# Kernel optimization log

Measured on AMD Instinct MI355X. Metric: run time of the kernel, lower is better.

Reference implementation:

```python
import jax, jax.numpy as jnp
import numpy as np

N_CAND = 10   # n_point_candidate
SIGMA = 1.0   # std threshold for vote filtering
EPS = 1e-6


def _get_pt_candidates(pcld, kpts_ofst, seg, cpt_ofst, k):
    # pcld [b,n,3]; kpts_ofst [b,n,8,3]; seg [b,n,1]; cpt_ofst [b,n,1,3]
    offsets = jnp.concatenate([kpts_ofst, cpt_ofst], axis=2)        # [b,n,9,3]
    scores = jnp.squeeze(seg, axis=-1)                              # [b,n]
    _, idx = jax.lax.top_k(scores, k)                               # [b,k] most confident points
    cands = pcld[:, :, None, :] + offsets                           # [b,n,9,3] candidate kpt positions
    cands = jnp.take_along_axis(cands, idx[:, :, None, None], axis=1)  # [b,k,9,3]
    return jnp.transpose(cands, (0, 2, 1, 3))                       # [b,9,k,3]


def _pts_clustering_with_std(kpts_cans, sigma=SIGMA):
    # kpts_cans [b,n_kpts,k,3]: keep candidates within sigma*std of the mean, average survivors
    mean = jnp.mean(kpts_cans, axis=2, keepdims=True)
    std = jnp.std(kpts_cans, axis=2, keepdims=True)
    inlier = jnp.all(jnp.abs(kpts_cans - mean) <= sigma * std, axis=-1)  # [b,n_kpts,k]
    w = inlier.astype(kpts_cans.dtype)[..., None]
    return jnp.sum(kpts_cans * w, axis=2) / (jnp.sum(w, axis=2) + EPS)   # [b,n_kpts,3]


def _rt_svd_transform(A, B, w):
    # Weighted Kabsch: find R,t with R @ A + t ~= B.  A,B [b,n,3]; w [n]
    wn = w / jnp.sum(w)
    cA = jnp.einsum('n,bnc->bc', wn, A)[:, None, :]                 # weighted centroids
    cB = jnp.einsum('n,bnc->bc', wn, B)[:, None, :]
    Am, Bm = A - cA, B - cB
    H = jnp.einsum('bni,n,bnj->bij', Am, w, Bm)                     # [b,3,3] cross-covariance
    U, S, Vh = jnp.linalg.svd(H)
    V = jnp.swapaxes(Vh, -1, -2)
    R0 = V @ jnp.swapaxes(U, -1, -2)
    flip = jnp.where(jnp.linalg.det(R0) < 0.0, -1.0, 1.0)           # reflection fix
    V = V.at[:, :, -1].multiply(flip[:, None])
    R = V @ jnp.swapaxes(U, -1, -2)                                 # [b,3,3]
    t = jnp.swapaxes(cB, -1, -2) - R @ jnp.swapaxes(cA, -1, -2)     # [b,3,1]
    return R, t


def setup_inputs() -> dict:
    key = jax.random.key(0)
    k1, k2, k3, k4, k5 = jax.random.split(key, 5)
    b, n, nk = 64, 12288, 8
    return {
        'pcld_input': jax.random.normal(k1, (b, n, 3), jnp.float32),
        'kpts_pre_input': jax.random.normal(k2, (b, n, nk, 3), jnp.float32),
        'cpt_pre_input': jax.random.normal(k3, (b, n, 1, 3), jnp.float32),
        'seg_pre_input': jax.random.uniform(k4, (b, n, 1), jnp.float32),
        'mesh_kpts_input': jax.random.normal(k5, (b, nk + 1, 3), jnp.float32),
    }


def reference(pcld_input, kpts_pre_input, cpt_pre_input, seg_pre_input, mesh_kpts_input):
    obj_kpts = _get_pt_candidates(pcld_input, kpts_pre_input, seg_pre_input, cpt_pre_input, N_CAND)
    kpts_voted = _pts_clustering_with_std(obj_kpts)                 # [b,9,3]
    n_pts = kpts_voted.shape[1]
    weights_vector = jnp.ones((n_pts,), dtype=kpts_voted.dtype)
    batch_R, batch_t = _rt_svd_transform(mesh_kpts_input, kpts_voted, weights_vector)
    batch_t = jnp.reshape(batch_t, (-1, 3))
    return batch_R, batch_t, kpts_voted
```

## Files before the change

kernel.cpp:

```cpp
#include <hip/hip_runtime.h>
#include <math.h>

typedef unsigned long long u64;
typedef unsigned int u32;

#define NB      64
#define NPTS    12288
#define KTOP    10
#define NKP     9
#define T       1024
#define CAND_MAX 128
#define THETA   0.997f

#define CHUNKS   4
#define TPB_A    768
#define CAP      64
#define WS_STRIDE 320

__device__ __forceinline__ u64 pack(float v, int idx) {
    return ((u64)__float_as_uint(v) << 32) | (u32)(~idx);
}
__device__ __forceinline__ int unpack_idx(u64 p) { return (int)(~(u32)p); }

__device__ __forceinline__ float rcp_fast(float x)  { return __builtin_amdgcn_rcpf(x); }
__device__ __forceinline__ float rsq_fast(float x)  { return __builtin_amdgcn_rsqf(x); }
__device__ __forceinline__ float sqrt_fast(float x) { return __builtin_amdgcn_sqrtf(x); }

__global__ __launch_bounds__(TPB_A)
void pose_onepass(const float* __restrict__ pcld,
                  const float* __restrict__ kpts,
                  const float* __restrict__ cpt,
                  const float* __restrict__ seg,
                  const float* __restrict__ mesh,
                  u32* __restrict__ ctr,
                  u64* __restrict__ wsd,
                  float* __restrict__ out)
{
    const int blk   = blockIdx.x;
    const int b     = blk >> 2;
    const int chunk = blk & 3;
    const int t     = threadIdx.x;
    const int lane  = t & 63;

    __shared__ u64    lc[CAP];
    __shared__ int    lcnt;
    __shared__ int    last_s;
    __shared__ u64    cand[CHUNKS * CAP];
    __shared__ int    cnts_s[CHUNKS];
    __shared__ int    n_s, bad_s;
    __shared__ int    topidx[KTOP];
    __shared__ float4 cands4[NKP][KTOP];
    __shared__ float  voted[NKP][3];
    __shared__ float  meshS[NKP * 3];

    if (t == 0) lcnt = 0;
    __syncthreads();

    const float4* segc4 = (const float4*)(seg + (size_t)b * NPTS) + (size_t)chunk * TPB_A;
    float4 a = segc4[t];
    const int base_idx = chunk * (TPB_A * 4) + t * 4;
    #pragma unroll
    for (int c = 0; c < 4; ++c) {
        float v = (c == 0) ? a.x : (c == 1) ? a.y : (c == 2) ? a.z : a.w;
        if (v >= THETA) {
            int slot = atomicAdd(&lcnt, 1);
            if (slot < CAP) lc[slot] = pack(v, base_idx + c);
        }
    }
    __syncthreads();

    u64* wb = wsd + (size_t)b * WS_STRIDE;
    if (t == 0) wb[chunk] = (u64)lcnt;
    int m = lcnt < CAP ? lcnt : CAP;
    if (t < m) wb[4 + chunk * CAP + t] = lc[t];
    __syncthreads();

    if (t == 0) {
        __threadfence();
        u32 old = atomicAdd(&ctr[b], 1u);
        if (old == 3u) __threadfence();
        last_s = (old == 3u) ? 1 : 0;
    }
    __syncthreads();
    if (!last_s) return;

    float meshv = 0.0f;
    if (t < NKP * 3) meshv = mesh[(size_t)b * (NKP * 3) + t];
    if (t < CHUNKS * CAP) cand[t] = wb[4 + t];
    if (t == 0) {
        int off = 0, badv = 0;
        #pragma unroll
        for (int c = 0; c < CHUNKS; ++c) {
            int cc = (int)wb[c];
            cnts_s[c] = cc < CAP ? cc : CAP;
            off += cc;
            if (cc > CAP) badv = 1;
        }
        n_s = off;
        bad_s = badv;
    }
    if (t < NKP * 3) meshS[t] = meshv;
    __syncthreads();

    const int n = n_s;
    const int bad = bad_s;

    if (!bad && n >= KTOP) {
        if (t < CHUNKS * CAP) {
            u64 my = cand[t];
            bool valid = (t & (CAP - 1)) < cnts_s[t >> 6];
            int r = 0;
            #pragma unroll
            for (int c2 = 0; c2 < CHUNKS; ++c2) {
                int cc = cnts_s[c2];
                for (int i2 = 0; i2 < cc; ++i2)
                    r += (cand[c2 * CAP + i2] > my) ? 1 : 0;
            }
            if (valid && r < KTOP) topidx[r] = unpack_idx(my);
        }
    } else if (t < 64) {
        const float* segb = seg + (size_t)b * NPTS;
        u64 loc[KTOP];
        #pragma unroll
        for (int j = 0; j < KTOP; ++j) loc[j] = 0;
        for (int i = lane; i < NPTS; i += 64) {
            u64 p = pack(segb[i], i);
            if (p > loc[KTOP - 1]) {
                loc[KTOP - 1] = p;
                #pragma unroll
                for (int j = KTOP - 1; j > 0; --j) {
                    if (loc[j] > loc[j - 1]) { u64 tmp = loc[j]; loc[j] = loc[j - 1]; loc[j - 1] = tmp; }
                }
            }
        }
        u64 cur = loc[0];
        #pragma unroll
        for (int k = 0; k < KTOP; ++k) {
            u64 w = cur;
            #pragma unroll
            for (int s = 1; s < 64; s <<= 1) {
                u64 o = __shfl_xor(w, s);
                w = o > w ? o : w;
            }
            if (lane == 0) topidx[k] = unpack_idx(w);
            if (cur == w) {
                #pragma unroll
                for (int i = 0; i + 1 < KTOP; ++i) loc[i] = loc[i + 1];
                loc[KTOP - 1] = 0;
                cur = loc[0];
            }
        }
    }
    __syncthreads();

    if (t < NKP * KTOP) {
        int j = t / KTOP;
        int i = t % KTOP;
        int p = topidx[i];
        size_t base = (size_t)b * NPTS + p;
        float px = pcld[base * 3 + 0], py = pcld[base * 3 + 1], pz = pcld[base * 3 + 2];
        float ox, oy, oz;
        if (j < 8) {
            size_t kb = (base * 8 + j) * 3;
            ox = kpts[kb + 0]; oy = kpts[kb + 1]; oz = kpts[kb + 2];
        } else {
            size_t cb = base * 3;
            ox = cpt[cb + 0]; oy = cpt[cb + 1]; oz = cpt[cb + 2];
        }
        cands4[j][i] = make_float4(px + ox, py + oy, pz + oz, 0.0f);
    }
    __syncthreads();

    if (t < NKP) {
        float4 c4[KTOP];
        #pragma unroll
        for (int i = 0; i < KTOP; ++i) c4[i] = cands4[t][i];

        float mean[3] = {0.f, 0.f, 0.f};
        #pragma unroll
        for (int i = 0; i < KTOP; ++i) {
            mean[0] += c4[i].x; mean[1] += c4[i].y; mean[2] += c4[i].z;
        }
        #pragma unroll
        for (int c = 0; c < 3; ++c) mean[c] *= (1.0f / KTOP);

        float var[3] = {0.f, 0.f, 0.f};
        #pragma unroll
        for (int i = 0; i < KTOP; ++i) {
            float d0 = c4[i].x - mean[0]; var[0] += d0 * d0;
            float d1 = c4[i].y - mean[1]; var[1] += d1 * d1;
            float d2 = c4[i].z - mean[2]; var[2] += d2 * d2;
        }
        float sd[3];
        #pragma unroll
        for (int c = 0; c < 3; ++c) sd[c] = sqrtf(var[c] * (1.0f / KTOP));

        float wsum = 0.f, acc[3] = {0.f, 0.f, 0.f};
        #pragma unroll
        for (int i = 0; i < KTOP; ++i) {
            bool in = (fabsf(c4[i].x - mean[0]) <= sd[0]) &&
                      (fabsf(c4[i].y - mean[1]) <= sd[1]) &&
                      (fabsf(c4[i].z - mean[2]) <= sd[2]);
            if (in) {
                wsum += 1.f;
                acc[0] += c4[i].x; acc[1] += c4[i].y; acc[2] += c4[i].z;
            }
        }
        float inv = 1.f / (wsum + 1e-6f);
        #pragma unroll
        for (int c = 0; c < 3; ++c) {
            float v = acc[c] * inv;
            voted[t][c] = v;
            out[NB * 9 + NB * 3 + ((size_t)b * NKP + t) * 3 + c] = v;
        }
    }
    __syncthreads();

    if (t == 0) {
        float A[NKP][3], Bv[NKP][3];
        float cA[3] = {0, 0, 0}, cB[3] = {0, 0, 0};
        for (int nn = 0; nn < NKP; ++nn) {
            for (int c = 0; c < 3; ++c) {
                A[nn][c]  = meshS[nn * 3 + c];
                Bv[nn][c] = voted[nn][c];
                cA[c] += A[nn][c];
                cB[c] += Bv[nn][c];
            }
        }
        for (int c = 0; c < 3; ++c) { cA[c] *= (1.0f / NKP); cB[c] *= (1.0f / NKP); }

        float H[3][3] = {{0,0,0},{0,0,0},{0,0,0}};
        for (int nn = 0; nn < NKP; ++nn)
            for (int i = 0; i < 3; ++i)
                for (int j = 0; j < 3; ++j)
                    H[i][j] += (A[nn][i] - cA[i]) * (Bv[nn][j] - cB[j]);

        float Km[3][3];
        for (int i = 0; i < 3; ++i)
            for (int j = 0; j < 3; ++j) {
                float s = 0;
                for (int l = 0; l < 3; ++l) s += H[l][i] * H[l][j];
                Km[i][j] = s;
            }

        float V[3][3] = {{1,0,0},{0,1,0},{0,0,1}};
        for (int sweep = 0; sweep < 5; ++sweep) {
            for (int p = 0; p < 2; ++p) {
                for (int q = p + 1; q < 3; ++q) {
                    float apq = Km[p][q];
                    float app = Km[p][p], aqq = Km[q][q];
                    if (fabsf(apq) <= 1e-12f * (fabsf(app) + fabsf(aqq)) || apq == 0.0f) continue;
                    float theta = (aqq - app) * rcp_fast(2.0f * apq);
                    float tj = ((theta >= 0.0f) ? 1.0f : -1.0f) *
                               rcp_fast(fabsf(theta) + sqrt_fast(theta * theta + 1.0f));
                    float cj = rsq_fast(tj * tj + 1.0f);
                    float sj = tj * cj;
                    for (int l = 0; l < 3; ++l) {
                        float klp = Km[l][p], klq = Km[l][q];
                        Km[l][p] = cj * klp - sj * klq;
                        Km[l][q] = sj * klp + cj * klq;
                    }
                    for (int l = 0; l < 3; ++l) {
                        float kpl = Km[p][l], kql = Km[q][l];
                        Km[p][l] = cj * kpl - sj * kql;
                        Km[q][l] = sj * kpl + cj * kql;
                    }
                    for (int l = 0; l < 3; ++l) {
                        float vlp = V[l][p], vlq = V[l][q];
                        V[l][p] = cj * vlp - sj * vlq;
                        V[l][q] = sj * vlp + cj * vlq;
                    }
                }
            }
        }

        float eig[3] = {Km[0][0], Km[1][1], Km[2][2]};
        int ord[3] = {0, 1, 2};
        if (eig[ord[0]] < eig[ord[1]]) { int tmp = ord[0]; ord[0] = ord[1]; ord[1] = tmp; }
        if (eig[ord[1]] < eig[ord[2]]) { int tmp = ord[1]; ord[1] = ord[2]; ord[2] = tmp; }
        if (eig[ord[0]] < eig[ord[1]]) { int tmp = ord[0]; ord[0] = ord[1]; ord[1] = tmp; }

        float detH =
            H[0][0] * (H[1][1] * H[2][2] - H[1][2] * H[2][1]) -
            H[0][1] * (H[1][0] * H[2][2] - H[1][2] * H[2][0]) +
            H[0][2] * (H[1][0] * H[2][1] - H[1][1] * H[2][0]);
        float dsign[3] = {1.0f, 1.0f, (detH < 0.0f) ? -1.0f : 1.0f};

        float R[3][3] = {{0,0,0},{0,0,0},{0,0,0}};
        for (int k = 0; k < 3; ++k) {
            int c = ord[k];
            float s = sqrt_fast(fmaxf(eig[c], 0.0f));
            float invs = rcp_fast(fmaxf(s, 1e-12f));
            float u[3];
            for (int l = 0; l < 3; ++l) {
                float a2 = 0;
                for (int mm = 0; mm < 3; ++mm) a2 += H[l][mm] * V[mm][c];
                u[l] = a2 * invs;
            }
            for (int r = 0; r < 3; ++r)
                for (int cc = 0; cc < 3; ++cc)
                    R[r][cc] += dsign[k] * V[r][c] * u[cc];
        }

        float tv[3];
        for (int c = 0; c < 3; ++c) {
            float a2 = 0;
            for (int mm = 0; mm < 3; ++mm) a2 += R[c][mm] * cA[mm];
            tv[c] = cB[c] - a2;
        }

        for (int r = 0; r < 3; ++r)
            for (int c = 0; c < 3; ++c)
                out[(size_t)b * 9 + r * 3 + c] = R[r][c];
        for (int c = 0; c < 3; ++c)
            out[NB * 9 + (size_t)b * 3 + c] = tv[c];
    }
}

__global__ __launch_bounds__(T)
void pose_fused(const float* __restrict__ pcld,
                const float* __restrict__ kpts,
                const float* __restrict__ cpt,
                const float* __restrict__ seg,
                const float* __restrict__ mesh,
                float* __restrict__ out)
{
    const int b = blockIdx.x;
    const int t = threadIdx.x;
    const int lane = t & 63;
    const int wid = t >> 6;

    __shared__ u64    cand[CAND_MAX];
    __shared__ int    cnt;
    __shared__ int    topidx[KTOP];
    __shared__ float4 cands4[NKP][KTOP];
    __shared__ float  voted[NKP][3];
    __shared__ float  meshS[NKP * 3];

    if (t == 0) cnt = 0;
    float meshv = 0.0f;
    if (t < NKP * 3) meshv = mesh[(size_t)b * (NKP * 3) + t];
    __syncthreads();

    const float4* segb4 = (const float4*)(seg + (size_t)b * NPTS);
    #pragma unroll
    for (int j = 0; j < 3; ++j) {
        int f4 = t + j * T;
        float4 a = segb4[f4];
        #pragma unroll
        for (int c = 0; c < 4; ++c) {
            float v = (c == 0) ? a.x : (c == 1) ? a.y : (c == 2) ? a.z : a.w;
            if (v >= THETA) {
                int slot = atomicAdd(&cnt, 1);
                if (slot < CAND_MAX) cand[slot] = pack(v, 4 * f4 + c);
            }
        }
    }
    if (t < NKP * 3) meshS[t] = meshv;
    __syncthreads();

    if (wid == 0) {
        int n = cnt;
        if (n >= KTOP && n <= CAND_MAX) {
            u64 my0 = (lane < n)      ? cand[lane]      : 0;
            u64 my1 = (lane + 64 < n) ? cand[lane + 64] : 0;
            int r0 = 0, r1 = 0;
            for (int i = 0; i < n; ++i) {
                u64 ci = cand[i];
                r0 += (ci > my0) ? 1 : 0;
                r1 += (ci > my1) ? 1 : 0;
            }
            if (lane < n && r0 < KTOP)      topidx[r0] = unpack_idx(my0);
            if (lane + 64 < n && r1 < KTOP) topidx[r1] = unpack_idx(my1);
        } else {
            const float* segb = seg + (size_t)b * NPTS;
            u64 loc[KTOP];
            #pragma unroll
            for (int j = 0; j < KTOP; ++j) loc[j] = 0;
            for (int i = lane; i < NPTS; i += 64) {
                u64 p = pack(segb[i], i);
                if (p > loc[KTOP - 1]) {
                    loc[KTOP - 1] = p;
                    #pragma unroll
                    for (int j = KTOP - 1; j > 0; --j) {
                        if (loc[j] > loc[j - 1]) { u64 tmp = loc[j]; loc[j] = loc[j - 1]; loc[j - 1] = tmp; }
                    }
                }
            }
            u64 cur = loc[0];
            #pragma unroll
            for (int k = 0; k < KTOP; ++k) {
                u64 w = cur;
                #pragma unroll
                for (int s = 1; s < 64; s <<= 1) {
                    u64 o = __shfl_xor(w, s);
                    w = o > w ? o : w;
                }
                if (lane == 0) topidx[k] = unpack_idx(w);
                if (cur == w) {
                    #pragma unroll
                    for (int i = 0; i + 1 < KTOP; ++i) loc[i] = loc[i + 1];
                    loc[KTOP - 1] = 0;
                    cur = loc[0];
                }
            }
        }
    }
    __syncthreads();

    if (t < NKP * KTOP) {
        int j = t / KTOP;
        int i = t % KTOP;
        int p = topidx[i];
        size_t base = (size_t)b * NPTS + p;
        float px = pcld[base * 3 + 0], py = pcld[base * 3 + 1], pz = pcld[base * 3 + 2];
        float ox, oy, oz;
        if (j < 8) {
            size_t kb = (base * 8 + j) * 3;
            ox = kpts[kb + 0]; oy = kpts[kb + 1]; oz = kpts[kb + 2];
        } else {
            size_t cb = base * 3;
            ox = cpt[cb + 0]; oy = cpt[cb + 1]; oz = cpt[cb + 2];
        }
        cands4[j][i] = make_float4(px + ox, py + oy, pz + oz, 0.0f);
    }
    __syncthreads();

    if (t < NKP) {
        float4 c4[KTOP];
        #pragma unroll
        for (int i = 0; i < KTOP; ++i) c4[i] = cands4[t][i];
        float mean[3] = {0.f, 0.f, 0.f};
        #pragma unroll
        for (int i = 0; i < KTOP; ++i) { mean[0] += c4[i].x; mean[1] += c4[i].y; mean[2] += c4[i].z; }
        #pragma unroll
        for (int c = 0; c < 3; ++c) mean[c] *= (1.0f / KTOP);
        float var[3] = {0.f, 0.f, 0.f};
        #pragma unroll
        for (int i = 0; i < KTOP; ++i) {
            float d0 = c4[i].x - mean[0]; var[0] += d0 * d0;
            float d1 = c4[i].y - mean[1]; var[1] += d1 * d1;
            float d2 = c4[i].z - mean[2]; var[2] += d2 * d2;
        }
        float sd[3];
        #pragma unroll
        for (int c = 0; c < 3; ++c) sd[c] = sqrtf(var[c] * (1.0f / KTOP));
        float wsum = 0.f, acc[3] = {0.f, 0.f, 0.f};
        #pragma unroll
        for (int i = 0; i < KTOP; ++i) {
            bool in = (fabsf(c4[i].x - mean[0]) <= sd[0]) &&
                      (fabsf(c4[i].y - mean[1]) <= sd[1]) &&
                      (fabsf(c4[i].z - mean[2]) <= sd[2]);
            if (in) { wsum += 1.f; acc[0] += c4[i].x; acc[1] += c4[i].y; acc[2] += c4[i].z; }
        }
        float inv = 1.f / (wsum + 1e-6f);
        #pragma unroll
        for (int c = 0; c < 3; ++c) {
            float v = acc[c] * inv;
            voted[t][c] = v;
            out[NB * 9 + NB * 3 + ((size_t)b * NKP + t) * 3 + c] = v;
        }
    }
    __syncthreads();

    if (t == 0) {
        float A[NKP][3], Bv[NKP][3];
        float cA[3] = {0, 0, 0}, cB[3] = {0, 0, 0};
        for (int nn = 0; nn < NKP; ++nn) {
            for (int c = 0; c < 3; ++c) {
                A[nn][c]  = meshS[nn * 3 + c];
                Bv[nn][c] = voted[nn][c];
                cA[c] += A[nn][c];
                cB[c] += Bv[nn][c];
            }
        }
        for (int c = 0; c < 3; ++c) { cA[c] *= (1.0f / NKP); cB[c] *= (1.0f / NKP); }
        float H[3][3] = {{0,0,0},{0,0,0},{0,0,0}};
        for (int nn = 0; nn < NKP; ++nn)
            for (int i = 0; i < 3; ++i)
                for (int j = 0; j < 3; ++j)
                    H[i][j] += (A[nn][i] - cA[i]) * (Bv[nn][j] - cB[j]);
        float Km[3][3];
        for (int i = 0; i < 3; ++i)
            for (int j = 0; j < 3; ++j) {
                float s = 0;
                for (int l = 0; l < 3; ++l) s += H[l][i] * H[l][j];
                Km[i][j] = s;
            }
        float V[3][3] = {{1,0,0},{0,1,0},{0,0,1}};
        for (int sweep = 0; sweep < 5; ++sweep) {
            for (int p = 0; p < 2; ++p) {
                for (int q = p + 1; q < 3; ++q) {
                    float apq = Km[p][q];
                    float app = Km[p][p], aqq = Km[q][q];
                    if (fabsf(apq) <= 1e-12f * (fabsf(app) + fabsf(aqq)) || apq == 0.0f) continue;
                    float theta = (aqq - app) * rcp_fast(2.0f * apq);
                    float tj = ((theta >= 0.0f) ? 1.0f : -1.0f) *
                               rcp_fast(fabsf(theta) + sqrt_fast(theta * theta + 1.0f));
                    float cj = rsq_fast(tj * tj + 1.0f);
                    float sj = tj * cj;
                    for (int l = 0; l < 3; ++l) {
                        float klp = Km[l][p], klq = Km[l][q];
                        Km[l][p] = cj * klp - sj * klq;
                        Km[l][q] = sj * klp + cj * klq;
                    }
                    for (int l = 0; l < 3; ++l) {
                        float kpl = Km[p][l], kql = Km[q][l];
                        Km[p][l] = cj * kpl - sj * kql;
                        Km[q][l] = sj * kpl + cj * kql;
                    }
                    for (int l = 0; l < 3; ++l) {
                        float vlp = V[l][p], vlq = V[l][q];
                        V[l][p] = cj * vlp - sj * vlq;
                        V[l][q] = sj * vlp + cj * vlq;
                    }
                }
            }
        }
        float eig[3] = {Km[0][0], Km[1][1], Km[2][2]};
        int ord[3] = {0, 1, 2};
        if (eig[ord[0]] < eig[ord[1]]) { int tmp = ord[0]; ord[0] = ord[1]; ord[1] = tmp; }
        if (eig[ord[1]] < eig[ord[2]]) { int tmp = ord[1]; ord[1] = ord[2]; ord[2] = tmp; }
        if (eig[ord[0]] < eig[ord[1]]) { int tmp = ord[0]; ord[0] = ord[1]; ord[1] = tmp; }
        float detH =
            H[0][0] * (H[1][1] * H[2][2] - H[1][2] * H[2][1]) -
            H[0][1] * (H[1][0] * H[2][2] - H[1][2] * H[2][0]) +
            H[0][2] * (H[1][0] * H[2][1] - H[1][1] * H[2][0]);
        float dsign[3] = {1.0f, 1.0f, (detH < 0.0f) ? -1.0f : 1.0f};
        float R[3][3] = {{0,0,0},{0,0,0},{0,0,0}};
        for (int k = 0; k < 3; ++k) {
            int c = ord[k];
            float s = sqrt_fast(fmaxf(eig[c], 0.0f));
            float invs = rcp_fast(fmaxf(s, 1e-12f));
            float u[3];
            for (int l = 0; l < 3; ++l) {
                float a2 = 0;
                for (int mm = 0; mm < 3; ++mm) a2 += H[l][mm] * V[mm][c];
                u[l] = a2 * invs;
            }
            for (int r = 0; r < 3; ++r)
                for (int cc = 0; cc < 3; ++cc)
                    R[r][cc] += dsign[k] * V[r][c] * u[cc];
        }
        float tv[3];
        for (int c = 0; c < 3; ++c) {
            float a2 = 0;
            for (int mm = 0; mm < 3; ++mm) a2 += R[c][mm] * cA[mm];
            tv[c] = cB[c] - a2;
        }
        for (int r = 0; r < 3; ++r)
            for (int c = 0; c < 3; ++c)
                out[(size_t)b * 9 + r * 3 + c] = R[r][c];
        for (int c = 0; c < 3; ++c)
            out[NB * 9 + (size_t)b * 3 + c] = tv[c];
    }
}

extern "C" void kernel_launch(void* const* d_in, const int* in_sizes, int n_in,
                              void* d_out, int out_size, void* d_ws, size_t ws_size,
                              hipStream_t stream) {
    const float* pcld = (const float*)d_in[0];
    const float* kpts = (const float*)d_in[1];
    const float* cpt  = (const float*)d_in[2];
    const float* seg  = (const float*)d_in[3];
    const float* mesh = (const float*)d_in[4];
    float* out = (float*)d_out;

    const size_t need = 256 + (size_t)NB * WS_STRIDE * sizeof(u64);
    if (d_ws != nullptr && ws_size >= need) {
        u32* ctr = (u32*)d_ws;
        u64* wsd = (u64*)((char*)d_ws + 256);
        hipMemsetAsync(d_ws, 0, NB * sizeof(u32), stream);
        pose_onepass<<<NB * CHUNKS, TPB_A, 0, stream>>>(pcld, kpts, cpt, seg, mesh, ctr, wsd, out);
    } else {
        pose_fused<<<NB, T, 0, stream>>>(pcld, kpts, cpt, seg, mesh, out);
    }
}
```

Measured before the change: 133.3 us.

## Split one-pass kernel into filter and solve kernels, dropping memset and atomic counter

Measured after the change: 119.0 us. 10.7% less time.

```diff
diff --git a/kernel.cpp b/kernel.cpp
--- a/kernel.cpp
+++ b/kernel.cpp
@@ -15,6 +15,7 @@
 #define CHUNKS   4
 #define TPB_A    768
 #define CAP      64
+#define TPB_B    256
 #define WS_STRIDE 320
 
 __device__ __forceinline__ u64 pack(float v, int idx) {
@@ -27,32 +28,15 @@
 __device__ __forceinline__ float sqrt_fast(float x) { return __builtin_amdgcn_sqrtf(x); }
 
 __global__ __launch_bounds__(TPB_A)
-void pose_onepass(const float* __restrict__ pcld,
-                  const float* __restrict__ kpts,
-                  const float* __restrict__ cpt,
-                  const float* __restrict__ seg,
-                  const float* __restrict__ mesh,
-                  u32* __restrict__ ctr,
-                  u64* __restrict__ wsd,
-                  float* __restrict__ out)
+void pose_filter(const float* __restrict__ seg, u64* __restrict__ ws)
 {
     const int blk   = blockIdx.x;
     const int b     = blk >> 2;
     const int chunk = blk & 3;
     const int t     = threadIdx.x;
-    const int lane  = t & 63;
-
-    __shared__ u64    lc[CAP];
-    __shared__ int    lcnt;
-    __shared__ int    last_s;
-    __shared__ u64    cand[CHUNKS * CAP];
-    __shared__ int    cnts_s[CHUNKS];
-    __shared__ int    n_s, bad_s;
-    __shared__ int    topidx[KTOP];
-    __shared__ float4 cands4[NKP][KTOP];
-    __shared__ float  voted[NKP][3];
-    __shared__ float  meshS[NKP * 3];
-
+
+    __shared__ u64 lc[CAP];
+    __shared__ int lcnt;
     if (t == 0) lcnt = 0;
     __syncthreads();
 
@@ -69,55 +53,62 @@
     }
     __syncthreads();
 
-    u64* wb = wsd + (size_t)b * WS_STRIDE;
+    u64* wb = ws + (size_t)b * WS_STRIDE;
     if (t == 0) wb[chunk] = (u64)lcnt;
     int m = lcnt < CAP ? lcnt : CAP;
     if (t < m) wb[4 + chunk * CAP + t] = lc[t];
-    __syncthreads();
-
-    if (t == 0) {
-        __threadfence();
-        u32 old = atomicAdd(&ctr[b], 1u);
-        if (old == 3u) __threadfence();
-        last_s = (old == 3u) ? 1 : 0;
-    }
-    __syncthreads();
-    if (!last_s) return;
+}
+
+__global__ __launch_bounds__(TPB_B)
+void pose_solve(const float* __restrict__ pcld,
+                const float* __restrict__ kpts,
+                const float* __restrict__ cpt,
+                const float* __restrict__ seg,
+                const float* __restrict__ mesh,
+                const u64*   __restrict__ ws,
+                float* __restrict__ out)
+{
+    const int b = blockIdx.x;
+    const int t = threadIdx.x;
+    const int lane = t & 63;
+
+    __shared__ u64    cand[CHUNKS * CAP];
+    __shared__ int    cntf_s[CHUNKS];
+    __shared__ int    topidx[KTOP];
+    __shared__ float4 cands4[NKP][KTOP];
+    __shared__ float  voted[NKP][3];
+    __shared__ float  meshS[NKP * 3];
+
+    const u64* wb = ws + (size_t)b * WS_STRIDE;
 
     float meshv = 0.0f;
     if (t < NKP * 3) meshv = mesh[(size_t)b * (NKP * 3) + t];
-    if (t < CHUNKS * CAP) cand[t] = wb[4 + t];
-    if (t == 0) {
-        int off = 0, badv = 0;
-        #pragma unroll
-        for (int c = 0; c < CHUNKS; ++c) {
-            int cc = (int)wb[c];
-            cnts_s[c] = cc < CAP ? cc : CAP;
-            off += cc;
-            if (cc > CAP) badv = 1;
-        }
-        n_s = off;
-        bad_s = badv;
-    }
+    cand[t] = wb[4 + t];
+    if (t < CHUNKS) cntf_s[t] = (int)wb[t];
     if (t < NKP * 3) meshS[t] = meshv;
     __syncthreads();
 
-    const int n = n_s;
-    const int bad = bad_s;
+    int cnts[CHUNKS];
+    int n = 0, bad = 0;
+    #pragma unroll
+    for (int c = 0; c < CHUNKS; ++c) {
+        int cc = cntf_s[c];
+        n += cc;
+        if (cc > CAP) bad = 1;
+        cnts[c] = cc < CAP ? cc : CAP;
+    }
 
     if (!bad && n >= KTOP) {
-        if (t < CHUNKS * CAP) {
-            u64 my = cand[t];
-            bool valid = (t & (CAP - 1)) < cnts_s[t >> 6];
-            int r = 0;
-            #pragma unroll
-            for (int c2 = 0; c2 < CHUNKS; ++c2) {
-                int cc = cnts_s[c2];
-                for (int i2 = 0; i2 < cc; ++i2)
-                    r += (cand[c2 * CAP + i2] > my) ? 1 : 0;
-            }
-            if (valid && r < KTOP) topidx[r] = unpack_idx(my);
-        }
+        u64 my = cand[t];
+        bool valid = (t & (CAP - 1)) < cnts[t >> 6];
+        int r = 0;
+        #pragma unroll
+        for (int c2 = 0; c2 < CHUNKS; ++c2) {
+            int cc = cnts[c2];
+            for (int i2 = 0; i2 < cc; ++i2)
+                r += (cand[c2 * CAP + i2] > my) ? 1 : 0;
+        }
+        if (valid && r < KTOP) topidx[r] = unpack_idx(my);
     } else if (t < 64) {
         const float* segb = seg + (size_t)b * NPTS;
         u64 loc[KTOP];
@@ -566,12 +557,11 @@
     const float* mesh = (const float*)d_in[4];
     float* out = (float*)d_out;
 
-    const size_t need = 256 + (size_t)NB * WS_STRIDE * sizeof(u64);
+    const size_t need = (size_t)NB * WS_STRIDE * sizeof(u64);
     if (d_ws != nullptr && ws_size >= need) {
-        u32* ctr = (u32*)d_ws;
-        u64* wsd = (u64*)((char*)d_ws + 256);
-        hipMemsetAsync(d_ws, 0, NB * sizeof(u32), stream);
-        pose_onepass<<<NB * CHUNKS, TPB_A, 0, stream>>>(pcld, kpts, cpt, seg, mesh, ctr, wsd, out);
+        u64* ws = (u64*)d_ws;
+        pose_filter<<<NB * CHUNKS, TPB_A, 0, stream>>>(seg, ws);
+        pose_solve<<<NB, TPB_B, 0, stream>>>(pcld, kpts, cpt, seg, mesh, ws, out);
     } else {
         pose_fused<<<NB, T, 0, stream>>>(pcld, kpts, cpt, seg, mesh, out);
     }
```
